# Kernel optimization log

Hardware: AMD Instinct MI355X
Metric: run time of the kernel (lower is better)

Reference implementation:

```python
import jax, jax.numpy as jnp
import numpy as np


def _species_mlp(x, W1, b1, W2, b2, W3, b3, W4, b4):
    # x: [S, A, F] per-species feature blocks; weights: [S, ...] per-species MLPs
    h = jax.nn.silu(jnp.einsum('saf,sfh->sah', x, W1) + b1[:, None, :])
    h = jax.nn.silu(jnp.einsum('sah,shk->sak', h, W2) + b2[:, None, :])
    h = jax.nn.silu(jnp.einsum('sak,skm->sam', h, W3) + b3[:, None, :])
    e = jnp.einsum('sam,smo->sao', h, W4) + b4[:, None, :]  # [S, A, 1]
    return e[..., 0]  # atomic energies [S, A]


def setup_inputs() -> dict:
    key = jax.random.key(0)
    ks = jax.random.split(key, 12)
    S, A, F, H = 4, 32768, 512, 256
    n_structures = 512
    w = 0.05  # keep activations in a sane range
    return {
        'features': jax.random.normal(ks[0], (S, A, F), dtype=jnp.float32),
        'struct_ids': jax.random.randint(ks[1], (S, A), 0, n_structures),
        'W1': jax.random.normal(ks[2], (S, F, H), dtype=jnp.float32) * w,
        'b1': jax.random.normal(ks[3], (S, H), dtype=jnp.float32) * w,
        'W2': jax.random.normal(ks[4], (S, H, H), dtype=jnp.float32) * w,
        'b2': jax.random.normal(ks[5], (S, H), dtype=jnp.float32) * w,
        'W3': jax.random.normal(ks[6], (S, H, H), dtype=jnp.float32) * w,
        'b3': jax.random.normal(ks[7], (S, H), dtype=jnp.float32) * w,
        'W4': jax.random.normal(ks[8], (S, H, 1), dtype=jnp.float32) * w,
        'b4': jax.random.normal(ks[9], (S, 1), dtype=jnp.float32) * w,
        'energy_shift': jax.random.normal(ks[10], (1,), dtype=jnp.float32),
        'n_structures': n_structures,
    }


def reference(features, struct_ids, W1, b1, W2, b2, W3, b3, W4, b4, energy_shift, n_structures):
    # per-species MLP over all blocks (the per-species gather is the block layout itself)
    atomic_energies = _species_mlp(features, W1, b1, W2, b2, W3, b3, W4, b4)  # [S, A]
    # index_add scatter of atomic energies into per-structure energies
    energies = jax.ops.segment_sum(
        atomic_energies.reshape(-1), struct_ids.reshape(-1), num_segments=n_structures
    )
    energies = energies + energy_shift[0]
    return energies
```

## Files before the change

kernel.cpp:

```cpp
#include <hip/hip_runtime.h>

typedef _Float16 f16x8 __attribute__((ext_vector_type(8)));
typedef _Float16 f16x4 __attribute__((ext_vector_type(4)));
typedef float f32x4 __attribute__((ext_vector_type(4)));

static constexpr int S = 4;
static constexpr int NATOMS = 32768;
static constexpr int FIN = 512;
static constexpr int H = 256;
static constexpr int BM = 64;
static constexpr int XSTR = 72;
static constexpr int HSTR = 264;
static constexpr int NSTRUCT = 512;
static constexpr int RBLK = 128;
static constexpr int APB = (S * NATOMS) / RBLK;

__global__ void pack_w(const float* __restrict__ W, _Float16* __restrict__ dst, int KT, int l1) {
    int idx = blockIdx.x * 256 + threadIdx.x;
    int j = idx & 7;
    int lane = (idx >> 3) & 63;
    int rest = idx >> 9;
    int kt = rest % KT;
    int t2 = rest / KT;
    int K = KT * 32;
    int k = kt * 32 + (lane >> 4) * 8 + j;
    int ntile = t2 & 15;
    int s = t2 >> 4;
    int n = ntile * 16 + (lane & 15);
    int p = l1 ? ((kt >> 1) * 4 + (kt & 1) * 2 + (ntile & 1))
               : (kt * 2 + (ntile & 1));
    size_t o = ((((size_t)(s * 8 + (ntile >> 1))) * (KT * 2) + p) * 64 + lane) * 8 + j;
    dst[o] = (_Float16)W[((size_t)s * K + k) * H + n];
}

__global__ __launch_bounds__(512, 4) void fused_mlp(
    const float* __restrict__ X,
    const _Float16* __restrict__ W1p, const _Float16* __restrict__ W2p,
    const _Float16* __restrict__ W3p,
    const float* __restrict__ b1, const float* __restrict__ b2,
    const float* __restrict__ b3,
    const float* __restrict__ W4, const float* __restrict__ b4,
    float* __restrict__ Eout)
{
    __shared__ _Float16 smem[BM * HSTR];
    __shared__ float e_lds[8][BM];

    const int s = blockIdx.y;
    const int tile = blockIdx.x;
    const int tid = threadIdx.x;
    const int rw = __builtin_amdgcn_readfirstlane(tid >> 6);
    const int lane = tid & 63;
    const int g = lane >> 4;
    const int mh = lane & 15;
    const int srow = tid >> 3;
    const int cq = tid & 7;

    const float* Xb = X + (size_t)(s * NATOMS + tile * BM) * FIN;
    _Float16* hb = smem;

    const _Float16* Wb1 = W1p + ((size_t)(s * 8 + rw)) * (32 * 512) + lane * 8;
    const _Float16* Wb2 = W2p + ((size_t)(s * 8 + rw)) * (16 * 512) + lane * 8;
    const _Float16* Wb3 = W3p + ((size_t)(s * 8 + rw)) * (16 * 512) + lane * 8;

    f32x4 acc[4][2];
#pragma unroll
    for (int i = 0; i < 4; ++i)
#pragma unroll
        for (int j = 0; j < 2; ++j)
            acc[i][j] = f32x4{0.f, 0.f, 0.f, 0.f};

    f32x4 ld[4][2];
    auto loadc = [&](int slot, int c) {
        const float* p = Xb + (size_t)srow * FIN + c * 64 + cq * 8;
        ld[slot][0] = *(const f32x4*)(p);
        ld[slot][1] = *(const f32x4*)(p + 4);
    };
    auto storec = [&](int slot, int c) {
        _Float16* xb = smem + (c % 3) * (BM * XSTR);
#pragma unroll
        for (int i = 0; i < 2; ++i) {
            f16x4 v;
#pragma unroll
            for (int j = 0; j < 4; ++j) v[j] = (_Float16)ld[slot][i][j];
            *(f16x4*)(xb + srow * XSTR + cq * 8 + i * 4) = v;
        }
    };
    auto l1mfma = [&](int c) {
        const _Float16* xb = smem + (c % 3) * (BM * XSTR);
#pragma unroll
        for (int ks = 0; ks < 2; ++ks) {
            f16x8 a[4];
#pragma unroll
            for (int mt = 0; mt < 4; ++mt)
                a[mt] = *(const f16x8*)(xb + (mt * 16 + mh) * XSTR + (ks * 4 + g) * 8);
            __builtin_amdgcn_s_setprio(1);
#pragma unroll
            for (int nt = 0; nt < 2; ++nt) {
                f16x8 b = *(const f16x8*)(Wb1 + (c * 4 + ks * 2 + nt) * 512);
#pragma unroll
                for (int mt = 0; mt < 4; ++mt)
                    acc[mt][nt] = __builtin_amdgcn_mfma_f32_16x16x32_f16(a[mt], b, acc[mt][nt], 0, 0, 0);
            }
            __builtin_amdgcn_s_setprio(0);
        }
    };

    loadc(0, 0);
    loadc(1, 1);
    loadc(2, 2);
    loadc(3, 3);
    storec(0, 0);
    asm volatile("s_waitcnt lgkmcnt(0)" ::: "memory");
    __builtin_amdgcn_s_barrier();
#pragma unroll
    for (int c = 0; c < 8; ++c) {
        if (c < 7) storec((c + 1) & 3, c + 1);
        if (c < 4) loadc(c & 3, c + 4);
        l1mfma(c);
        asm volatile("s_waitcnt lgkmcnt(0)" ::: "memory");
        __builtin_amdgcn_s_barrier();
    }
    __syncthreads();

    {
        float bv[2];
#pragma unroll
        for (int nt = 0; nt < 2; ++nt) bv[nt] = b1[s * H + rw * 32 + nt * 16 + mh];
#pragma unroll
        for (int mt = 0; mt < 4; ++mt)
#pragma unroll
            for (int nt = 0; nt < 2; ++nt)
#pragma unroll
                for (int r = 0; r < 4; ++r) {
                    float v = acc[mt][nt][r] + bv[nt];
                    v = __fdividef(v, 1.f + __expf(-v));
                    hb[(mt * 16 + g * 4 + r) * HSTR + rw * 32 + nt * 16 + mh] = (_Float16)v;
                    acc[mt][nt][r] = 0.f;
                }
    }
    __syncthreads();

    for (int l = 0; l < 2; ++l) {
        const _Float16* Wb = l ? Wb3 : Wb2;
#pragma unroll
        for (int ks = 0; ks < 8; ++ks) {
            f16x8 a[4];
#pragma unroll
            for (int mt = 0; mt < 4; ++mt)
                a[mt] = *(const f16x8*)(hb + (mt * 16 + mh) * HSTR + ks * 32 + g * 8);
            __builtin_amdgcn_s_setprio(1);
#pragma unroll
            for (int nt = 0; nt < 2; ++nt) {
                f16x8 b = *(const f16x8*)(Wb + (ks * 2 + nt) * 512);
#pragma unroll
                for (int mt = 0; mt < 4; ++mt)
                    acc[mt][nt] = __builtin_amdgcn_mfma_f32_16x16x32_f16(a[mt], b, acc[mt][nt], 0, 0, 0);
            }
            __builtin_amdgcn_s_setprio(0);
        }
        __syncthreads();
        if (l == 0) {
            float bv[2];
#pragma unroll
            for (int nt = 0; nt < 2; ++nt) bv[nt] = b2[s * H + rw * 32 + nt * 16 + mh];
#pragma unroll
            for (int mt = 0; mt < 4; ++mt)
#pragma unroll
                for (int nt = 0; nt < 2; ++nt)
#pragma unroll
                    for (int r = 0; r < 4; ++r) {
                        float v = acc[mt][nt][r] + bv[nt];
                        v = __fdividef(v, 1.f + __expf(-v));
                        hb[(mt * 16 + g * 4 + r) * HSTR + rw * 32 + nt * 16 + mh] = (_Float16)v;
                        acc[mt][nt][r] = 0.f;
                    }
            __syncthreads();
        }
    }

    {
        float bv[2], w4v[2];
#pragma unroll
        for (int nt = 0; nt < 2; ++nt) {
            int col = rw * 32 + nt * 16 + mh;
            bv[nt] = b3[s * H + col];
            w4v[nt] = W4[s * H + col];
        }
#pragma unroll
        for (int mt = 0; mt < 4; ++mt)
#pragma unroll
            for (int r = 0; r < 4; ++r) {
                float v = 0.f;
#pragma unroll
                for (int nt = 0; nt < 2; ++nt) {
                    float h = acc[mt][nt][r] + bv[nt];
                    h = __fdividef(h, 1.f + __expf(-h));
                    v += h * w4v[nt];
                }
                v += __shfl_xor(v, 1);
                v += __shfl_xor(v, 2);
                v += __shfl_xor(v, 4);
                v += __shfl_xor(v, 8);
                if (mh == r) e_lds[rw][mt * 16 + g * 4 + r] = v;
            }
    }
    __syncthreads();
    if (tid < BM) {
        float e = b4[s];
#pragma unroll
        for (int j = 0; j < 8; ++j) e += e_lds[j][tid];
        Eout[(size_t)s * NATOMS + tile * BM + tid] = e;
    }
}

__global__ __launch_bounds__(256) void reduce1(
    const float* __restrict__ E, const int* __restrict__ ids,
    float* __restrict__ partials)
{
    __shared__ float tbl[NSTRUCT];
    const int b = blockIdx.x;
    const int tid = threadIdx.x;
    tbl[tid] = 0.f;
    tbl[tid + 256] = 0.f;
    __syncthreads();
    const int base = b * APB;
#pragma unroll
    for (int i = 0; i < APB / 256; ++i) {
        int a = base + i * 256 + tid;
        atomicAdd(&tbl[ids[a]], E[a]);
    }
    __syncthreads();
    partials[(size_t)b * NSTRUCT + tid] = tbl[tid];
    partials[(size_t)b * NSTRUCT + tid + 256] = tbl[tid + 256];
}

__global__ __launch_bounds__(512) void reduce2(
    const float* __restrict__ partials, const float* __restrict__ shift,
    float* __restrict__ out)
{
    const int i = threadIdx.x;
    float v = shift[0];
#pragma unroll 8
    for (int b = 0; b < RBLK; ++b) v += partials[(size_t)b * NSTRUCT + i];
    out[i] = v;
}

extern "C" void kernel_launch(void* const* d_in, const int* in_sizes, int n_in,
                              void* d_out, int out_size, void* d_ws, size_t ws_size,
                              hipStream_t stream) {
    const float* X   = (const float*)d_in[0];
    const int*   ids = (const int*)d_in[1];
    const float* W1  = (const float*)d_in[2];
    const float* b1  = (const float*)d_in[3];
    const float* W2  = (const float*)d_in[4];
    const float* b2  = (const float*)d_in[5];
    const float* W3  = (const float*)d_in[6];
    const float* b3  = (const float*)d_in[7];
    const float* W4  = (const float*)d_in[8];
    const float* b4  = (const float*)d_in[9];
    const float* shift = (const float*)d_in[10];

    _Float16* W1p = (_Float16*)d_ws;
    _Float16* W2p = W1p + (size_t)S * 8 * 32 * 512;
    _Float16* W3p = W2p + (size_t)S * 8 * 16 * 512;
    float* E = (float*)(W3p + (size_t)S * 8 * 16 * 512);
    float* partials = E + (size_t)S * NATOMS;

    pack_w<<<2048, 256, 0, stream>>>(W1, W1p, 16, 1);
    pack_w<<<1024, 256, 0, stream>>>(W2, W2p, 8, 0);
    pack_w<<<1024, 256, 0, stream>>>(W3, W3p, 8, 0);

    dim3 grid(NATOMS / BM, S);
    fused_mlp<<<grid, 512, 0, stream>>>(X, W1p, W2p, W3p, b1, b2, b3, W4, b4, E);

    reduce1<<<RBLK, 256, 0, stream>>>(E, ids, partials);
    reduce2<<<1, 512, 0, stream>>>(partials, shift, (float*)d_out);
}
```

Before: 149.7 us.

## Use 128-row tiles with 2x4 warp grid and 64-wide N per warp

Doubles the atom tile to 128 rows and arranges the 8 waves as a 2x4 grid, so each wave computes a 64x64 output block instead of 64x32. Each weight fragment loaded from global memory now feeds twice as many MFMAs, halving weight traffic per atom. The layer-1 X pipeline switches to 32-column chunks with a 3-stage ring, and the weight packing is rearranged to match. In exchange each wave needs twice the accumulator registers, so launch bounds drop to 3 blocks per CU and the grid halves.

```diff
diff --git a/kernel.cpp b/kernel.cpp
--- a/kernel.cpp
+++ b/kernel.cpp
@@ -8,14 +8,14 @@
 static constexpr int NATOMS = 32768;
 static constexpr int FIN = 512;
 static constexpr int H = 256;
-static constexpr int BM = 64;
-static constexpr int XSTR = 72;
+static constexpr int BM = 128;
+static constexpr int XSTR = 36;
 static constexpr int HSTR = 264;
 static constexpr int NSTRUCT = 512;
 static constexpr int RBLK = 128;
 static constexpr int APB = (S * NATOMS) / RBLK;
 
-__global__ void pack_w(const float* __restrict__ W, _Float16* __restrict__ dst, int KT, int l1) {
+__global__ void pack_w(const float* __restrict__ W, _Float16* __restrict__ dst, int KT) {
     int idx = blockIdx.x * 256 + threadIdx.x;
     int j = idx & 7;
     int lane = (idx >> 3) & 63;
@@ -27,13 +27,12 @@
     int ntile = t2 & 15;
     int s = t2 >> 4;
     int n = ntile * 16 + (lane & 15);
-    int p = l1 ? ((kt >> 1) * 4 + (kt & 1) * 2 + (ntile & 1))
-               : (kt * 2 + (ntile & 1));
-    size_t o = ((((size_t)(s * 8 + (ntile >> 1))) * (KT * 2) + p) * 64 + lane) * 8 + j;
+    int p = kt * 4 + (ntile & 3);
+    size_t o = ((((size_t)(s * 4 + (ntile >> 2))) * (KT * 4) + p) * 64 + lane) * 8 + j;
     dst[o] = (_Float16)W[((size_t)s * K + k) * H + n];
 }
 
-__global__ __launch_bounds__(512, 4) void fused_mlp(
+__global__ __launch_bounds__(512, 3) void fused_mlp(
     const float* __restrict__ X,
     const _Float16* __restrict__ W1p, const _Float16* __restrict__ W2p,
     const _Float16* __restrict__ W3p,
@@ -43,35 +42,37 @@
     float* __restrict__ Eout)
 {
     __shared__ _Float16 smem[BM * HSTR];
-    __shared__ float e_lds[8][BM];
+    __shared__ float e_lds[4][BM];
 
     const int s = blockIdx.y;
     const int tile = blockIdx.x;
     const int tid = threadIdx.x;
     const int rw = __builtin_amdgcn_readfirstlane(tid >> 6);
+    const int wm = rw >> 2;
+    const int wn = rw & 3;
     const int lane = tid & 63;
     const int g = lane >> 4;
     const int mh = lane & 15;
-    const int srow = tid >> 3;
-    const int cq = tid & 7;
+    const int srow = tid >> 2;
+    const int cq = tid & 3;
 
     const float* Xb = X + (size_t)(s * NATOMS + tile * BM) * FIN;
     _Float16* hb = smem;
 
-    const _Float16* Wb1 = W1p + ((size_t)(s * 8 + rw)) * (32 * 512) + lane * 8;
-    const _Float16* Wb2 = W2p + ((size_t)(s * 8 + rw)) * (16 * 512) + lane * 8;
-    const _Float16* Wb3 = W3p + ((size_t)(s * 8 + rw)) * (16 * 512) + lane * 8;
-
-    f32x4 acc[4][2];
+    const _Float16* Wb1 = W1p + ((size_t)(s * 4 + wn)) * (64 * 512) + lane * 8;
+    const _Float16* Wb2 = W2p + ((size_t)(s * 4 + wn)) * (32 * 512) + lane * 8;
+    const _Float16* Wb3 = W3p + ((size_t)(s * 4 + wn)) * (32 * 512) + lane * 8;
+
+    f32x4 acc[4][4];
 #pragma unroll
     for (int i = 0; i < 4; ++i)
 #pragma unroll
-        for (int j = 0; j < 2; ++j)
+        for (int j = 0; j < 4; ++j)
             acc[i][j] = f32x4{0.f, 0.f, 0.f, 0.f};
 
-    f32x4 ld[4][2];
+    f32x4 ld[3][2];
     auto loadc = [&](int slot, int c) {
-        const float* p = Xb + (size_t)srow * FIN + c * 64 + cq * 8;
+        const float* p = Xb + (size_t)srow * FIN + c * 32 + cq * 8;
         ld[slot][0] = *(const f32x4*)(p);
         ld[slot][1] = *(const f32x4*)(p + 4);
     };
@@ -87,91 +88,87 @@
     };
     auto l1mfma = [&](int c) {
         const _Float16* xb = smem + (c % 3) * (BM * XSTR);
-#pragma unroll
-        for (int ks = 0; ks < 2; ++ks) {
+        f16x8 a[4];
+#pragma unroll
+        for (int mt = 0; mt < 4; ++mt)
+            a[mt] = *(const f16x8*)(xb + (wm * 64 + mt * 16 + mh) * XSTR + g * 8);
+        __builtin_amdgcn_s_setprio(1);
+#pragma unroll
+        for (int nt = 0; nt < 4; ++nt) {
+            f16x8 b = *(const f16x8*)(Wb1 + (c * 4 + nt) * 512);
+#pragma unroll
+            for (int mt = 0; mt < 4; ++mt)
+                acc[mt][nt] = __builtin_amdgcn_mfma_f32_16x16x32_f16(a[mt], b, acc[mt][nt], 0, 0, 0);
+        }
+        __builtin_amdgcn_s_setprio(0);
+    };
+
+    loadc(0, 0);
+    loadc(1, 1);
+    loadc(2, 2);
+    storec(0, 0);
+    asm volatile("s_waitcnt lgkmcnt(0)" ::: "memory");
+    __builtin_amdgcn_s_barrier();
+#pragma unroll
+    for (int c = 0; c < 16; ++c) {
+        if (c < 15) storec((c + 1) % 3, c + 1);
+        if (c < 13) loadc(c % 3, c + 3);
+        l1mfma(c);
+        asm volatile("s_waitcnt lgkmcnt(0)" ::: "memory");
+        __builtin_amdgcn_s_barrier();
+    }
+    __syncthreads();
+
+    {
+        float bv[4];
+#pragma unroll
+        for (int nt = 0; nt < 4; ++nt) bv[nt] = b1[s * H + wn * 64 + nt * 16 + mh];
+#pragma unroll
+        for (int mt = 0; mt < 4; ++mt)
+#pragma unroll
+            for (int nt = 0; nt < 4; ++nt)
+#pragma unroll
+                for (int r = 0; r < 4; ++r) {
+                    float v = acc[mt][nt][r] + bv[nt];
+                    v = __fdividef(v, 1.f + __expf(-v));
+                    hb[(wm * 64 + mt * 16 + g * 4 + r) * HSTR + wn * 64 + nt * 16 + mh] = (_Float16)v;
+                    acc[mt][nt][r] = 0.f;
+                }
+    }
+    __syncthreads();
+
+    for (int l = 0; l < 2; ++l) {
+        const _Float16* Wb = l ? Wb3 : Wb2;
+#pragma unroll
+        for (int ks = 0; ks < 8; ++ks) {
             f16x8 a[4];
 #pragma unroll
             for (int mt = 0; mt < 4; ++mt)
-                a[mt] = *(const f16x8*)(xb + (mt * 16 + mh) * XSTR + (ks * 4 + g) * 8);
+                a[mt] = *(const f16x8*)(hb + (wm * 64 + mt * 16 + mh) * HSTR + ks * 32 + g * 8);
             __builtin_amdgcn_s_setprio(1);
 #pragma unroll
-            for (int nt = 0; nt < 2; ++nt) {
-                f16x8 b = *(const f16x8*)(Wb1 + (c * 4 + ks * 2 + nt) * 512);
+            for (int nt = 0; nt < 4; ++nt) {
+                f16x8 b = *(const f16x8*)(Wb + (ks * 4 + nt) * 512);
 #pragma unroll
                 for (int mt = 0; mt < 4; ++mt)
                     acc[mt][nt] = __builtin_amdgcn_mfma_f32_16x16x32_f16(a[mt], b, acc[mt][nt], 0, 0, 0);
             }
             __builtin_amdgcn_s_setprio(0);
         }
-    };
-
-    loadc(0, 0);
-    loadc(1, 1);
-    loadc(2, 2);
-    loadc(3, 3);
-    storec(0, 0);
-    asm volatile("s_waitcnt lgkmcnt(0)" ::: "memory");
-    __builtin_amdgcn_s_barrier();
-#pragma unroll
-    for (int c = 0; c < 8; ++c) {
-        if (c < 7) storec((c + 1) & 3, c + 1);
-        if (c < 4) loadc(c & 3, c + 4);
-        l1mfma(c);
-        asm volatile("s_waitcnt lgkmcnt(0)" ::: "memory");
-        __builtin_amdgcn_s_barrier();
-    }
-    __syncthreads();
-
-    {
-        float bv[2];
-#pragma unroll
-        for (int nt = 0; nt < 2; ++nt) bv[nt] = b1[s * H + rw * 32 + nt * 16 + mh];
-#pragma unroll
-        for (int mt = 0; mt < 4; ++mt)
-#pragma unroll
-            for (int nt = 0; nt < 2; ++nt)
-#pragma unroll
-                for (int r = 0; r < 4; ++r) {
-                    float v = acc[mt][nt][r] + bv[nt];
-                    v = __fdividef(v, 1.f + __expf(-v));
-                    hb[(mt * 16 + g * 4 + r) * HSTR + rw * 32 + nt * 16 + mh] = (_Float16)v;
-                    acc[mt][nt][r] = 0.f;
-                }
-    }
-    __syncthreads();
-
-    for (int l = 0; l < 2; ++l) {
-        const _Float16* Wb = l ? Wb3 : Wb2;
-#pragma unroll
-        for (int ks = 0; ks < 8; ++ks) {
-            f16x8 a[4];
-#pragma unroll
-            for (int mt = 0; mt < 4; ++mt)
-                a[mt] = *(const f16x8*)(hb + (mt * 16 + mh) * HSTR + ks * 32 + g * 8);
-            __builtin_amdgcn_s_setprio(1);
-#pragma unroll
-            for (int nt = 0; nt < 2; ++nt) {
-                f16x8 b = *(const f16x8*)(Wb + (ks * 2 + nt) * 512);
-#pragma unroll
-                for (int mt = 0; mt < 4; ++mt)
-                    acc[mt][nt] = __builtin_amdgcn_mfma_f32_16x16x32_f16(a[mt], b, acc[mt][nt], 0, 0, 0);
-            }
-            __builtin_amdgcn_s_setprio(0);
-        }
         __syncthreads();
         if (l == 0) {
-            float bv[2];
-#pragma unroll
-            for (int nt = 0; nt < 2; ++nt) bv[nt] = b2[s * H + rw * 32 + nt * 16 + mh];
+            float bv[4];
+#pragma unroll
+            for (int nt = 0; nt < 4; ++nt) bv[nt] = b2[s * H + wn * 64 + nt * 16 + mh];
 #pragma unroll
             for (int mt = 0; mt < 4; ++mt)
 #pragma unroll
-                for (int nt = 0; nt < 2; ++nt)
+                for (int nt = 0; nt < 4; ++nt)
 #pragma unroll
                     for (int r = 0; r < 4; ++r) {
                         float v = acc[mt][nt][r] + bv[nt];
                         v = __fdividef(v, 1.f + __expf(-v));
-                        hb[(mt * 16 + g * 4 + r) * HSTR + rw * 32 + nt * 16 + mh] = (_Float16)v;
+                        hb[(wm * 64 + mt * 16 + g * 4 + r) * HSTR + wn * 64 + nt * 16 + mh] = (_Float16)v;
                         acc[mt][nt][r] = 0.f;
                     }
             __syncthreads();
@@ -179,10 +176,10 @@
     }
 
     {
-        float bv[2], w4v[2];
-#pragma unroll
-        for (int nt = 0; nt < 2; ++nt) {
-            int col = rw * 32 + nt * 16 + mh;
+        float bv[4], w4v[4];
+#pragma unroll
+        for (int nt = 0; nt < 4; ++nt) {
+            int col = wn * 64 + nt * 16 + mh;
             bv[nt] = b3[s * H + col];
             w4v[nt] = W4[s * H + col];
         }
@@ -192,7 +189,7 @@
             for (int r = 0; r < 4; ++r) {
                 float v = 0.f;
 #pragma unroll
-                for (int nt = 0; nt < 2; ++nt) {
+                for (int nt = 0; nt < 4; ++nt) {
                     float h = acc[mt][nt][r] + bv[nt];
                     h = __fdividef(h, 1.f + __expf(-h));
                     v += h * w4v[nt];
@@ -201,14 +198,12 @@
                 v += __shfl_xor(v, 2);
                 v += __shfl_xor(v, 4);
                 v += __shfl_xor(v, 8);
-                if (mh == r) e_lds[rw][mt * 16 + g * 4 + r] = v;
+                if (mh == r) e_lds[wn][wm * 64 + mt * 16 + g * 4 + r] = v;
             }
     }
     __syncthreads();
     if (tid < BM) {
-        float e = b4[s];
-#pragma unroll
-        for (int j = 0; j < 8; ++j) e += e_lds[j][tid];
+        float e = b4[s] + e_lds[0][tid] + e_lds[1][tid] + e_lds[2][tid] + e_lds[3][tid];
         Eout[(size_t)s * NATOMS + tile * BM + tid] = e;
     }
 }
@@ -261,14 +256,14 @@
     const float* shift = (const float*)d_in[10];
 
     _Float16* W1p = (_Float16*)d_ws;
-    _Float16* W2p = W1p + (size_t)S * 8 * 32 * 512;
-    _Float16* W3p = W2p + (size_t)S * 8 * 16 * 512;
-    float* E = (float*)(W3p + (size_t)S * 8 * 16 * 512);
+    _Float16* W2p = W1p + (size_t)S * 4 * 64 * 512;
+    _Float16* W3p = W2p + (size_t)S * 4 * 32 * 512;
+    float* E = (float*)(W3p + (size_t)S * 4 * 32 * 512);
     float* partials = E + (size_t)S * NATOMS;
 
-    pack_w<<<2048, 256, 0, stream>>>(W1, W1p, 16, 1);
-    pack_w<<<1024, 256, 0, stream>>>(W2, W2p, 8, 0);
-    pack_w<<<1024, 256, 0, stream>>>(W3, W3p, 8, 0);
+    pack_w<<<2048, 256, 0, stream>>>(W1, W1p, 16);
+    pack_w<<<1024, 256, 0, stream>>>(W2, W2p, 8);
+    pack_w<<<1024, 256, 0, stream>>>(W3, W3p, 8);
 
     dim3 grid(NATOMS / BM, S);
     fused_mlp<<<grid, 512, 0, stream>>>(X, W1p, W2p, W3p, b1, b2, b3, W4, b4, E);
```

Measured after the change: 155.9 us. 1.04x slower.
